# Kernel optimization log

Hardware: AMD Instinct MI355X
Metric: run time of the kernel (lower is better)

Reference implementation:

```python
import jax, jax.numpy as jnp
import numpy as np

N_BLOCKS = 5
D_HIDDEN = 512
D_LATENT = 512
NUM_FREQ = 10
IMG_H = IMG_W = 128


@jax.custom_vjp
def trunc_exp(x):
    return jnp.exp(x)

def _te_fwd(x):
    return jnp.exp(x), x

def _te_bwd(x, g):
    return (g * jnp.exp(jnp.clip(x, -15.0, 15.0)),)

trunc_exp.defvjp(_te_fwd, _te_bwd)


def setup_inputs() -> dict:
    key = jax.random.key(0)
    ks = jax.random.split(key, 12)
    cam, ray, samp = 2, 1024, 48
    world_xyz = jax.random.normal(ks[0], (cam, ray, samp, 3), jnp.float32) * 0.5
    world_xyz = world_xyz.at[..., 2].add(2.5)  # keep points in front of identity camera
    c2w = jnp.tile(jnp.eye(4, dtype=jnp.float32), (cam, 1, 1))
    k_mat = jnp.tile(jnp.array([[128.0, 0.0, 64.0], [0.0, 128.0, 64.0], [0.0, 0.0, 1.0]], jnp.float32), (cam, 1, 1))
    features = jax.random.normal(ks[1], (cam, D_LATENT, IMG_H, IMG_W), jnp.float32)
    s = 0.02
    d_in = 3 + 3 * 2 * NUM_FREQ  # 63
    return {
        'world_xyz': world_xyz,
        'c2w': c2w,
        'k_mat': k_mat,
        'features': features,
        'lin_in_w': jax.random.normal(ks[2], (d_in, D_HIDDEN), jnp.float32) * s,
        'lin_in_b': jnp.zeros((D_HIDDEN,), jnp.float32),
        'lin_z_w': jax.random.normal(ks[3], (N_BLOCKS, D_LATENT, D_HIDDEN), jnp.float32) * s,
        'lin_z_b': jnp.zeros((N_BLOCKS, D_HIDDEN), jnp.float32),
        'fc0_w': jax.random.normal(ks[4], (N_BLOCKS, D_HIDDEN, D_HIDDEN), jnp.float32) * s,
        'fc0_b': jnp.zeros((N_BLOCKS, D_HIDDEN), jnp.float32),
        'fc1_w': jax.random.normal(ks[5], (N_BLOCKS, D_HIDDEN, D_HIDDEN), jnp.float32) * s,
        'fc1_b': jnp.zeros((N_BLOCKS, D_HIDDEN), jnp.float32),
        'lin_out_w': jax.random.normal(ks[6], (D_HIDDEN, 1), jnp.float32) * s,
        'lin_out_b': jnp.zeros((1,), jnp.float32),
    }


def _bilinear(feat, uv):
    # feat: [C, H, W]; uv: [N, 2] pixel coords. Bilinear, border padding, align_corners=True.
    Hd, Wd = feat.shape[1], feat.shape[2]
    x = jnp.clip(uv[:, 0], 0.0, Wd - 1.0)
    y = jnp.clip(uv[:, 1], 0.0, Hd - 1.0)
    x0 = jnp.floor(x); y0 = jnp.floor(y)
    x0i = x0.astype(jnp.int32); y0i = y0.astype(jnp.int32)
    x1i = jnp.minimum(x0i + 1, Wd - 1); y1i = jnp.minimum(y0i + 1, Hd - 1)
    wx = x - x0; wy = y - y0
    f00 = feat[:, y0i, x0i]; f01 = feat[:, y0i, x1i]
    f10 = feat[:, y1i, x0i]; f11 = feat[:, y1i, x1i]
    out = (f00 * ((1 - wx) * (1 - wy)) + f01 * (wx * (1 - wy)) +
           f10 * ((1 - wx) * wy) + f11 * (wx * wy))
    return out.T  # [N, C]


def _forward(world_xyz, c2w, k_mat, features, lin_in_w, lin_in_b, lin_z_w, lin_z_b,
             fc0_w, fc0_b, fc1_w, fc1_b, lin_out_w, lin_out_b):
    B, R, S, _ = world_xyz.shape
    pts = world_xyz.reshape(B, R * S, 3)
    # world -> camera (w2c = inverse of rigid c2w)
    rot = c2w[:, :3, :3]
    trans = c2w[:, :3, 3]
    cam_xyz = jnp.einsum('bji,bnj->bni', rot, pts - trans[:, None])  # R^T (p - t)
    # project with intrinsics
    uvw = jnp.einsum('bij,bnj->bni', k_mat, cam_xyz)
    z = uvw[..., 2:3]
    z = jnp.where(jnp.abs(z) < 1e-6, 1e-6, z)
    uv = uvw[..., :2] / z  # [B, N, 2] pixel coords
    aligned = jax.vmap(_bilinear)(features, uv)  # [B, N, C]
    # NeRF positional encoding (include_input=True, freqs 2^0..2^9, scaled by 2*pi)
    freqs = 2.0 ** jnp.arange(NUM_FREQ, dtype=jnp.float32)
    scaled = (2.0 * jnp.pi) * cam_xyz[..., None] * freqs  # [B, N, 3, F]
    scaled = scaled.reshape(B, R * S, 3 * NUM_FREQ)
    enc = jnp.concatenate([cam_xyz, jnp.sin(scaled), jnp.cos(scaled)], axis=-1)  # [B, N, 63]
    # ResnetFC: lin_in then residual blocks with latent injection
    h = enc @ lin_in_w + lin_in_b
    for i in range(N_BLOCKS):
        h = h + aligned @ lin_z_w[i] + lin_z_b[i]
        net = jax.nn.relu(h) @ fc0_w[i] + fc0_b[i]
        dx = jax.nn.relu(net) @ fc1_w[i] + fc1_b[i]
        h = h + dx
    sigma = jax.nn.relu(h) @ lin_out_w + lin_out_b  # [B, N, 1]
    return trunc_exp(sigma).reshape(B, R, S, 1)


def reference(world_xyz, c2w, k_mat, features, lin_in_w, lin_in_b, lin_z_w, lin_z_b,
              fc0_w, fc0_b, fc1_w, fc1_b, lin_out_w, lin_out_b):
    return _forward(world_xyz, c2w, k_mat, features, lin_in_w, lin_in_b, lin_z_w, lin_z_b,
                    fc0_w, fc0_b, fc1_w, fc1_b, lin_out_w, lin_out_b)
```

## Files before the change

kernel.cpp:

```cpp
#include <hip/hip_runtime.h>

typedef __bf16 bf16_t;
typedef bf16_t bf16x8 __attribute__((ext_vector_type(8)));
typedef float f32x4 __attribute__((ext_vector_type(4)));
typedef unsigned short u16;

#define P_TOTAL 98304
#define PTS_PER_BATCH 49152

__device__ __forceinline__ u16 f2bs(float f){ bf16_t b=(bf16_t)f; return __builtin_bit_cast(u16,b); }

__device__ __forceinline__ void bar_lds(){
  asm volatile("s_waitcnt lgkmcnt(0)" ::: "memory");
  __builtin_amdgcn_s_barrier();
  __builtin_amdgcn_sched_barrier(0);
}

__global__ void k_wtrans15(const float* __restrict__ lz, const float* __restrict__ f0,
                           const float* __restrict__ f1, u16* __restrict__ dst){
  int kt = blockIdx.x, ns = blockIdx.y, z = blockIdx.z;
  const float* src = (z<5) ? (lz + (size_t)z*262144)
                   : (z<10 ? (f0 + (size_t)(z-5)*262144)
                           : (f1 + (size_t)(z-10)*262144));
  u16* d = dst + (size_t)z*262144 + (size_t)(ns*16 + kt)*1024;
  int l = threadIdx.x;
  int col = ns*32 + (l&15);
  int kr  = kt*32 + (l>>4)*8;
  #pragma unroll
  for (int nt=0;nt<2;nt++){
    bf16x8 o;
    #pragma unroll
    for (int j=0;j<8;j++) o[j] = (bf16_t)src[(size_t)(kr+j)*512 + col + nt*16];
    *(bf16x8*)(d + nt*512 + l*8) = o;
  }
}

__global__ void k_wtrans_in(const float* __restrict__ w, u16* __restrict__ dst){
  int kt = blockIdx.x, ns = blockIdx.y;
  u16* d = dst + (size_t)(ns*2 + kt)*1024;
  int l = threadIdx.x;
  int col = ns*32 + (l&15);
  int kr  = kt*32 + (l>>4)*8;
  #pragma unroll
  for (int nt=0;nt<2;nt++){
    bf16x8 o;
    #pragma unroll
    for (int j=0;j<8;j++){
      int k = kr + j;
      o[j] = (k < 63) ? (bf16_t)w[(size_t)k*512 + col + nt*16] : (bf16_t)0.f;
    }
    *(bf16x8*)(d + nt*512 + l*8) = o;
  }
}

__global__ void k_featT(const float* __restrict__ feat, u16* __restrict__ featT){
  int x = threadIdx.x;
  int c8 = blockIdx.x*8;
  int y = blockIdx.y, b = blockIdx.z;
  float v[8];
  #pragma unroll
  for (int j=0;j<8;j++)
    v[j] = feat[(((size_t)(b*512 + c8 + j))*128 + y)*128 + x];
  bf16x8 o;
  #pragma unroll
  for (int j=0;j<8;j++) o[j] = (bf16_t)v[j];
  *(bf16x8*)(featT + (((size_t)(b*128 + y))*128 + x)*512 + c8) = o;
}

__global__ __launch_bounds__(1024) void k_points(
    const float* __restrict__ world, const float* __restrict__ c2w,
    const float* __restrict__ kmat, const u16* __restrict__ featT,
    u16* __restrict__ alignedF, u16* __restrict__ encF){
  __shared__ u16 act[16*520];
  __shared__ u16 encs[16*72];
  int wid = threadIdx.x >> 6, lane = threadIdx.x & 63;
  int p0 = blockIdx.x*16;
  int gp = p0 + wid;
  int b = gp / PTS_PER_BATCH;
  const float* wp = world + (size_t)gp*3;
  float px = wp[0], py = wp[1], pz = wp[2];
  const float* cw = c2w + b*16;
  float dx = px - cw[3], dy = py - cw[7], dz = pz - cw[11];
  float cx = cw[0]*dx + cw[4]*dy + cw[8]*dz;
  float cy = cw[1]*dx + cw[5]*dy + cw[9]*dz;
  float cz = cw[2]*dx + cw[6]*dy + cw[10]*dz;
  const float* km = kmat + b*9;
  float u0 = km[0]*cx + km[1]*cy + km[2]*cz;
  float v0 = km[3]*cx + km[4]*cy + km[5]*cz;
  float zz = km[6]*cx + km[7]*cy + km[8]*cz;
  if (fabsf(zz) < 1e-6f) zz = 1e-6f;
  float uu = u0/zz, vv = v0/zz;
  float xf = fminf(fmaxf(uu, 0.f), 127.f);
  float yf = fminf(fmaxf(vv, 0.f), 127.f);
  float x0f = floorf(xf), y0f = floorf(yf);
  int x0 = (int)x0f, y0 = (int)y0f;
  int x1 = min(x0+1,127), y1 = min(y0+1,127);
  float wx = xf - x0f, wy = yf - y0f;
  float w00 = (1.f-wx)*(1.f-wy), w01 = wx*(1.f-wy), w10 = (1.f-wx)*wy, w11 = wx*wy;
  size_t fb = (size_t)b*128*128*512;
  int c8 = lane*8;
  const bf16x8 t00 = *(const bf16x8*)(featT + fb + (size_t)(y0*128+x0)*512 + c8);
  const bf16x8 t01 = *(const bf16x8*)(featT + fb + (size_t)(y0*128+x1)*512 + c8);
  const bf16x8 t10 = *(const bf16x8*)(featT + fb + (size_t)(y1*128+x0)*512 + c8);
  const bf16x8 t11 = *(const bf16x8*)(featT + fb + (size_t)(y1*128+x1)*512 + c8);
  bf16x8 o;
  #pragma unroll
  for (int j=0;j<8;j++){
    float r = (float)t00[j]*w00 + (float)t01[j]*w01 + (float)t10[j]*w10 + (float)t11[j]*w11;
    o[j] = (bf16_t)r;
  }
  *(bf16x8*)&act[wid*520 + lane*8] = o;
  float cam[3] = {cx, cy, cz};
  float e;
  if (lane < 3) e = cam[lane];
  else if (lane < 33){
    int i = (lane-3)/10, f = (lane-3)%10;
    e = sinf(6.2831855f * cam[i] * (float)(1<<f));
  } else if (lane < 63){
    int i = (lane-33)/10, f = (lane-33)%10;
    e = cosf(6.2831855f * cam[i] * (float)(1<<f));
  } else e = 0.f;
  encs[wid*72 + lane] = f2bs(e);
  __syncthreads();
  int t = threadIdx.x;
  int g = blockIdx.x & 3;
  size_t blk = (size_t)(blockIdx.x >> 2);
  {
    int kt = t>>6, lo = t&63, fm = lo&15, fk8 = lo>>4;
    bf16x8 v = *(const bf16x8*)&act[fm*520 + kt*32 + fk8*8];
    *(bf16x8*)(alignedF + blk*32768 + (size_t)(kt*4+g)*512 + lo*8) = v;
  }
  if (t < 128){
    int kt = t>>6, lo = t&63, fm = lo&15, fk8 = lo>>4;
    bf16x8 v = *(const bf16x8*)&encs[fm*72 + kt*32 + fk8*8];
    *(bf16x8*)(encF + blk*4096 + (size_t)(kt*4+g)*512 + lo*8) = v;
  }
}


#define MFMA_BF16 __builtin_amdgcn_mfma_f32_16x16x32_bf16

template<int NK>
__device__ __forceinline__ void gemm3(const u16* sB, const u16* __restrict__ apS,
                                      const u16* __restrict__ apN,
                                      int l, f32x4 (&acc)[4][4], bf16x8 (&a)[2][4]){
  const u16* bp = sB + l*8;
  bf16x8 br[2][4];
  #pragma unroll
  for (int bt=0; bt<4; ++bt) br[0][bt] = *(const bf16x8*)(bp + bt*512);
  #pragma unroll 1
  for (int kb=0; kb<NK/2-1; ++kb){
    #pragma unroll
    for (int d=0; d<2; ++d){
      const int kt = kb*2 + d;
      #pragma unroll
      for (int bt=0; bt<4; ++bt)
        br[d^1][bt] = *(const bf16x8*)(bp + (kt+1)*2048 + bt*512);
      #pragma unroll
      for (int bt=0; bt<4; ++bt){
        acc[bt][0] = MFMA_BF16(a[d][0], br[d][bt], acc[bt][0], 0,0,0);
        acc[bt][1] = MFMA_BF16(a[d][1], br[d][bt], acc[bt][1], 0,0,0);
        acc[bt][2] = MFMA_BF16(a[d][2], br[d][bt], acc[bt][2], 0,0,0);
        acc[bt][3] = MFMA_BF16(a[d][3], br[d][bt], acc[bt][3], 0,0,0);
      }
      #pragma unroll
      for (int nt=0; nt<4; ++nt)
        a[d][nt] = *(const bf16x8*)(apS + (nt>>1)*(NK*1024) + (kt+2)*1024 + (nt&1)*512);
    }
  }
  #pragma unroll
  for (int d=0; d<2; ++d){
    if (d == 0){
      #pragma unroll
      for (int bt=0; bt<4; ++bt)
        br[1][bt] = *(const bf16x8*)(bp + (NK-1)*2048 + bt*512);
    }
    #pragma unroll
    for (int bt=0; bt<4; ++bt){
      acc[bt][0] = MFMA_BF16(a[d][0], br[d][bt], acc[bt][0], 0,0,0);
      acc[bt][1] = MFMA_BF16(a[d][1], br[d][bt], acc[bt][1], 0,0,0);
      acc[bt][2] = MFMA_BF16(a[d][2], br[d][bt], acc[bt][2], 0,0,0);
      acc[bt][3] = MFMA_BF16(a[d][3], br[d][bt], acc[bt][3], 0,0,0);
    }
    #pragma unroll
    for (int nt=0; nt<4; ++nt)
      a[d][nt] = *(const bf16x8*)(apN + (nt>>1)*16384 + d*1024 + (nt&1)*512);
  }
}

__device__ __forceinline__ void add_bias2(const float* __restrict__ bias, int wn64, int rq,
                                          f32x4 (&acc)[4][4]){
  #pragma unroll
  for (int nt=0; nt<4; ++nt){
    f32x4 bv = *(const f32x4*)&bias[wn64 + nt*16 + rq];
    #pragma unroll
    for (int bt=0; bt<4; ++bt)
      #pragma unroll
      for (int r=0; r<4; ++r)
        acc[bt][nt][r] += bv[r];
  }
}

__device__ __forceinline__ void write_relu3(u16* dst, int w, int fm, int fk8,
                                            f32x4 (&acc)[4][4]){
  u16* base = dst + w*4096 + (fk8>>1)*128 + fm*8 + (fk8&1)*4;
  #pragma unroll
  for (int bt=0; bt<4; ++bt)
    #pragma unroll
    for (int nt=0; nt<4; ++nt){
      u16 p0 = f2bs(fmaxf(acc[bt][nt][0], 0.f));
      u16 p1 = f2bs(fmaxf(acc[bt][nt][1], 0.f));
      u16 p2 = f2bs(fmaxf(acc[bt][nt][2], 0.f));
      u16 p3 = f2bs(fmaxf(acc[bt][nt][3], 0.f));
      uint2 v;
      v.x = (unsigned)p0 | ((unsigned)p1 << 16);
      v.y = (unsigned)p2 | ((unsigned)p3 << 16);
      *(uint2*)(base + (nt>>1)*2048 + (nt&1)*256 + bt*512) = v;
    }
}

__global__ __launch_bounds__(512, 2) void k_net(
    const u16* __restrict__ alignedF, const u16* __restrict__ encF,
    const u16* __restrict__ wtin, const float* __restrict__ b_in,
    const u16* __restrict__ wts, const float* __restrict__ bz,
    const float* __restrict__ b0, const float* __restrict__ b1,
    const float* __restrict__ wout, const float* __restrict__ bout,
    float* __restrict__ out)
{
  __shared__ u16 bufA[32768];
  __shared__ u16 bufB[32768];
  const int t = threadIdx.x, w = t>>6, l = t&63;
  const int wn64 = w*64, fm = l&15, fk8 = l>>4, rq = (l>>4)*4;

  uint4 sa[8];
  const uint4* srcA = (const uint4*)(alignedF + (size_t)blockIdx.x*32768);
  #pragma unroll
  for (int j=0;j<8;j++) sa[j] = srcA[j*512 + t];
  uint4 sb = *((const uint4*)(encF + (size_t)blockIdx.x*4096) + t);

  const u16* apE = wtin + (size_t)w*4096 + l*8;
  bf16x8 afr[2][4];
  #pragma unroll
  for (int d=0; d<2; ++d)
    #pragma unroll
    for (int nt=0; nt<4; ++nt)
      afr[d][nt] = *(const bf16x8*)(apE + (nt>>1)*2048 + d*1024 + (nt&1)*512);

  #pragma unroll
  for (int j=0;j<8;j++) *((uint4*)bufA + j*512 + t) = sa[j];
  *((uint4*)bufB + t) = sb;
  bar_lds();

  const u16* apz0 = wts + (size_t)w*32768 + l*8;
  f32x4 h[4][4] = {};
  gemm3<2>(bufB, apE, apz0, l, h, afr);
  add_bias2(b_in, wn64, rq, h);

  #pragma unroll 1
  for (int i=0;i<5;i++){
    const u16* apz  = wts + (size_t)i*262144      + (size_t)w*32768 + l*8;
    const u16* apf0 = wts + (size_t)(5+i)*262144  + (size_t)w*32768 + l*8;
    const u16* apf1 = wts + (size_t)(10+i)*262144 + (size_t)w*32768 + l*8;
    const u16* apzn = (i<4) ? (wts + (size_t)(i+1)*262144 + (size_t)w*32768 + l*8) : apE;

    gemm3<16>(bufA, apz, apf0, l, h, afr);
    add_bias2(bz + i*512, wn64, rq, h);
    bar_lds();
    write_relu3(bufB, w, fm, fk8, h);
    bar_lds();
    f32x4 acc[4][4] = {};
    gemm3<16>(bufB, apf0, apf1, l, acc, afr);
    add_bias2(b0 + i*512, wn64, rq, acc);
    bar_lds();
    write_relu3(bufB, w, fm, fk8, acc);
    bar_lds();
    gemm3<16>(bufB, apf1, apzn, l, h, afr);
    add_bias2(b1 + i*512, wn64, rq, h);
  }

  float s[4];
  {
    #pragma unroll
    for (int bt=0; bt<4; ++bt) s[bt] = 0.f;
    #pragma unroll
    for (int nt=0; nt<4; ++nt){
      f32x4 wv = *(const f32x4*)&wout[wn64 + nt*16 + rq];
      #pragma unroll
      for (int bt=0; bt<4; ++bt)
        #pragma unroll
        for (int r=0; r<4; ++r)
          s[bt] += fmaxf(h[bt][nt][r], 0.f) * wv[r];
    }
  }
  #pragma unroll
  for (int bt=0; bt<4; ++bt){
    s[bt] += __shfl_xor(s[bt], 16, 64);
    s[bt] += __shfl_xor(s[bt], 32, 64);
  }
  bar_lds();
  float* red = (float*)bufB;
  if (l < 16){
    #pragma unroll
    for (int bt=0; bt<4; ++bt)
      red[w*64 + bt*16 + l] = s[bt];
  }
  bar_lds();
  if (t < 64){
    float a = bout[0];
    #pragma unroll
    for (int wv=0; wv<8; wv++) a += red[wv*64 + t];
    out[blockIdx.x*64 + t] = expf(a);
  }
}

extern "C" void kernel_launch(void* const* d_in, const int* in_sizes, int n_in,
                              void* d_out, int out_size, void* d_ws, size_t ws_size,
                              hipStream_t stream) {
  const float* world = (const float*)d_in[0];
  const float* c2w   = (const float*)d_in[1];
  const float* kmat  = (const float*)d_in[2];
  const float* feat  = (const float*)d_in[3];
  const float* w_in  = (const float*)d_in[4];
  const float* b_in  = (const float*)d_in[5];
  const float* w_z   = (const float*)d_in[6];
  const float* b_z   = (const float*)d_in[7];
  const float* w_f0  = (const float*)d_in[8];
  const float* b_f0  = (const float*)d_in[9];
  const float* w_f1  = (const float*)d_in[10];
  const float* b_f1  = (const float*)d_in[11];
  const float* w_out = (const float*)d_in[12];
  const float* b_out = (const float*)d_in[13];
  float* out = (float*)d_out;
  char* ws = (char*)d_ws;

  size_t off = 0;
  u16* wts   = (u16*)(ws + off); off += (size_t)15*262144*2;
  u16* wtin  = (u16*)(ws + off); off += (size_t)512*64*2;
  u16* featT = (u16*)(ws + off); off += (size_t)2*128*128*512*2;
  u16* alignedF = (u16*)(ws + off); off += (size_t)P_TOTAL*512*2;
  u16* encF  = (u16*)(ws + off); off += (size_t)P_TOTAL*64*2;

  k_wtrans15<<<dim3(16,16,15), 64, 0, stream>>>(w_z, w_f0, w_f1, wts);
  k_wtrans_in<<<dim3(2,16,1), 64, 0, stream>>>(w_in, wtin);
  k_featT<<<dim3(64,128,2), 128, 0, stream>>>(feat, featT);
  k_points<<<dim3(P_TOTAL/16), 1024, 0, stream>>>(world, c2w, kmat, featT, alignedF, encF);
  k_net<<<dim3(P_TOTAL/64), 512, 0, stream>>>(alignedF, encF, wtin, b_in, wts,
      b_z, b_f0, b_f1, w_out, b_out, out);
}
```

Before: 839.5 us.

## Split MLP across 16 waves per block with staggered K order and MFMA priority

Doubles the k_net block to 1024 threads so each of 16 waves owns 32 output columns instead of 64, which halves per-wave accumulators and weight fragments. Each half of the waves starts its K loop at a different offset, so they read different LDS rows and weight rows and contend less. MFMA groups are wrapped in s_setprio to favour matrix issue. The cost is more barrier participants per block and less register reuse per wave. Launch bounds of 1024 threads with 4 blocks per CU may not fit alongside 128KB of LDS per block.

```diff
diff --git a/kernel.cpp b/kernel.cpp
--- a/kernel.cpp
+++ b/kernel.cpp
@@ -141,58 +141,103 @@
 #define MFMA_BF16 __builtin_amdgcn_mfma_f32_16x16x32_bf16
 
 template<int NK>
-__device__ __forceinline__ void gemm3(const u16* sB, const u16* __restrict__ apS,
-                                      const u16* __restrict__ apN,
-                                      int l, f32x4 (&acc)[4][4], bf16x8 (&a)[2][4]){
+__device__ __forceinline__ void gemm4(const u16* sB, const u16* __restrict__ apS,
+                                      const u16* __restrict__ apN, int l, int START,
+                                      f32x4 (&acc)[4][2], bf16x8 (&a)[2][2]){
   const u16* bp = sB + l*8;
-  bf16x8 br[2][4];
-  #pragma unroll
-  for (int bt=0; bt<4; ++bt) br[0][bt] = *(const bf16x8*)(bp + bt*512);
+  constexpr int M = NK - 1;
+  int c0 = START & M;
+  bf16x8 br0 = *(const bf16x8*)(bp + c0*2048);
+  bf16x8 br1 = *(const bf16x8*)(bp + c0*2048 + 512);
+  bf16x8 br2 = *(const bf16x8*)(bp + c0*2048 + 1024);
+  bf16x8 br3 = *(const bf16x8*)(bp + c0*2048 + 1536);
   #pragma unroll 1
-  for (int kb=0; kb<NK/2-1; ++kb){
-    #pragma unroll
-    for (int d=0; d<2; ++d){
-      const int kt = kb*2 + d;
-      #pragma unroll
-      for (int bt=0; bt<4; ++bt)
-        br[d^1][bt] = *(const bf16x8*)(bp + (kt+1)*2048 + bt*512);
-      #pragma unroll
-      for (int bt=0; bt<4; ++bt){
-        acc[bt][0] = MFMA_BF16(a[d][0], br[d][bt], acc[bt][0], 0,0,0);
-        acc[bt][1] = MFMA_BF16(a[d][1], br[d][bt], acc[bt][1], 0,0,0);
-        acc[bt][2] = MFMA_BF16(a[d][2], br[d][bt], acc[bt][2], 0,0,0);
-        acc[bt][3] = MFMA_BF16(a[d][3], br[d][bt], acc[bt][3], 0,0,0);
-      }
-      #pragma unroll
-      for (int nt=0; nt<4; ++nt)
-        a[d][nt] = *(const bf16x8*)(apS + (nt>>1)*(NK*1024) + (kt+2)*1024 + (nt&1)*512);
-    }
-  }
-  #pragma unroll
-  for (int d=0; d<2; ++d){
-    if (d == 0){
-      #pragma unroll
-      for (int bt=0; bt<4; ++bt)
-        br[1][bt] = *(const bf16x8*)(bp + (NK-1)*2048 + bt*512);
-    }
-    #pragma unroll
-    for (int bt=0; bt<4; ++bt){
-      acc[bt][0] = MFMA_BF16(a[d][0], br[d][bt], acc[bt][0], 0,0,0);
-      acc[bt][1] = MFMA_BF16(a[d][1], br[d][bt], acc[bt][1], 0,0,0);
-      acc[bt][2] = MFMA_BF16(a[d][2], br[d][bt], acc[bt][2], 0,0,0);
-      acc[bt][3] = MFMA_BF16(a[d][3], br[d][bt], acc[bt][3], 0,0,0);
-    }
-    #pragma unroll
-    for (int nt=0; nt<4; ++nt)
-      a[d][nt] = *(const bf16x8*)(apN + (nt>>1)*16384 + d*1024 + (nt&1)*512);
-  }
-}
-
-__device__ __forceinline__ void add_bias2(const float* __restrict__ bias, int wn64, int rq,
-                                          f32x4 (&acc)[4][4]){
-  #pragma unroll
-  for (int nt=0; nt<4; ++nt){
-    f32x4 bv = *(const f32x4*)&bias[wn64 + nt*16 + rq];
+  for (int ib=0; ib<NK/2-1; ++ib){
+    {
+      const int i = 2*ib;
+      __builtin_amdgcn_s_setprio(1);
+      acc[0][0] = MFMA_BF16(a[0][0], br0, acc[0][0], 0,0,0);
+      acc[0][1] = MFMA_BF16(a[0][1], br0, acc[0][1], 0,0,0);
+      acc[1][0] = MFMA_BF16(a[0][0], br1, acc[1][0], 0,0,0);
+      acc[1][1] = MFMA_BF16(a[0][1], br1, acc[1][1], 0,0,0);
+      acc[2][0] = MFMA_BF16(a[0][0], br2, acc[2][0], 0,0,0);
+      acc[2][1] = MFMA_BF16(a[0][1], br2, acc[2][1], 0,0,0);
+      acc[3][0] = MFMA_BF16(a[0][0], br3, acc[3][0], 0,0,0);
+      acc[3][1] = MFMA_BF16(a[0][1], br3, acc[3][1], 0,0,0);
+      __builtin_amdgcn_s_setprio(0);
+      int cn = (START + i + 1) & M;
+      br0 = *(const bf16x8*)(bp + cn*2048);
+      br1 = *(const bf16x8*)(bp + cn*2048 + 512);
+      br2 = *(const bf16x8*)(bp + cn*2048 + 1024);
+      br3 = *(const bf16x8*)(bp + cn*2048 + 1536);
+      int ca = (START + i + 2) & M;
+      a[0][0] = *(const bf16x8*)(apS + ca*1024);
+      a[0][1] = *(const bf16x8*)(apS + ca*1024 + 512);
+    }
+    {
+      const int i = 2*ib + 1;
+      __builtin_amdgcn_s_setprio(1);
+      acc[0][0] = MFMA_BF16(a[1][0], br0, acc[0][0], 0,0,0);
+      acc[0][1] = MFMA_BF16(a[1][1], br0, acc[0][1], 0,0,0);
+      acc[1][0] = MFMA_BF16(a[1][0], br1, acc[1][0], 0,0,0);
+      acc[1][1] = MFMA_BF16(a[1][1], br1, acc[1][1], 0,0,0);
+      acc[2][0] = MFMA_BF16(a[1][0], br2, acc[2][0], 0,0,0);
+      acc[2][1] = MFMA_BF16(a[1][1], br2, acc[2][1], 0,0,0);
+      acc[3][0] = MFMA_BF16(a[1][0], br3, acc[3][0], 0,0,0);
+      acc[3][1] = MFMA_BF16(a[1][1], br3, acc[3][1], 0,0,0);
+      __builtin_amdgcn_s_setprio(0);
+      int cn = (START + i + 1) & M;
+      br0 = *(const bf16x8*)(bp + cn*2048);
+      br1 = *(const bf16x8*)(bp + cn*2048 + 512);
+      br2 = *(const bf16x8*)(bp + cn*2048 + 1024);
+      br3 = *(const bf16x8*)(bp + cn*2048 + 1536);
+      int ca = (START + i + 2) & M;
+      a[1][0] = *(const bf16x8*)(apS + ca*1024);
+      a[1][1] = *(const bf16x8*)(apS + ca*1024 + 512);
+    }
+  }
+  {
+    __builtin_amdgcn_s_setprio(1);
+    acc[0][0] = MFMA_BF16(a[0][0], br0, acc[0][0], 0,0,0);
+    acc[0][1] = MFMA_BF16(a[0][1], br0, acc[0][1], 0,0,0);
+    acc[1][0] = MFMA_BF16(a[0][0], br1, acc[1][0], 0,0,0);
+    acc[1][1] = MFMA_BF16(a[0][1], br1, acc[1][1], 0,0,0);
+    acc[2][0] = MFMA_BF16(a[0][0], br2, acc[2][0], 0,0,0);
+    acc[2][1] = MFMA_BF16(a[0][1], br2, acc[2][1], 0,0,0);
+    acc[3][0] = MFMA_BF16(a[0][0], br3, acc[3][0], 0,0,0);
+    acc[3][1] = MFMA_BF16(a[0][1], br3, acc[3][1], 0,0,0);
+    __builtin_amdgcn_s_setprio(0);
+    int cn = (START + NK - 1) & M;
+    br0 = *(const bf16x8*)(bp + cn*2048);
+    br1 = *(const bf16x8*)(bp + cn*2048 + 512);
+    br2 = *(const bf16x8*)(bp + cn*2048 + 1024);
+    br3 = *(const bf16x8*)(bp + cn*2048 + 1536);
+    int ca = START & 15;
+    a[0][0] = *(const bf16x8*)(apN + ca*1024);
+    a[0][1] = *(const bf16x8*)(apN + ca*1024 + 512);
+  }
+  {
+    __builtin_amdgcn_s_setprio(1);
+    acc[0][0] = MFMA_BF16(a[1][0], br0, acc[0][0], 0,0,0);
+    acc[0][1] = MFMA_BF16(a[1][1], br0, acc[0][1], 0,0,0);
+    acc[1][0] = MFMA_BF16(a[1][0], br1, acc[1][0], 0,0,0);
+    acc[1][1] = MFMA_BF16(a[1][1], br1, acc[1][1], 0,0,0);
+    acc[2][0] = MFMA_BF16(a[1][0], br2, acc[2][0], 0,0,0);
+    acc[2][1] = MFMA_BF16(a[1][1], br2, acc[2][1], 0,0,0);
+    acc[3][0] = MFMA_BF16(a[1][0], br3, acc[3][0], 0,0,0);
+    acc[3][1] = MFMA_BF16(a[1][1], br3, acc[3][1], 0,0,0);
+    __builtin_amdgcn_s_setprio(0);
+    int ca = (START + 1) & 15;
+    a[1][0] = *(const bf16x8*)(apN + ca*1024);
+    a[1][1] = *(const bf16x8*)(apN + ca*1024 + 512);
+  }
+}
+
+__device__ __forceinline__ void add_bias4(const float* __restrict__ bias, int wn32, int rq,
+                                          f32x4 (&acc)[4][2]){
+  #pragma unroll
+  for (int nt=0; nt<2; ++nt){
+    f32x4 bv = *(const f32x4*)&bias[wn32 + nt*16 + rq];
     #pragma unroll
     for (int bt=0; bt<4; ++bt)
       #pragma unroll
@@ -201,13 +246,13 @@
   }
 }
 
-__device__ __forceinline__ void write_relu3(u16* dst, int w, int fm, int fk8,
-                                            f32x4 (&acc)[4][4]){
-  u16* base = dst + w*4096 + (fk8>>1)*128 + fm*8 + (fk8&1)*4;
+__device__ __forceinline__ void write_relu4(u16* dst, int w, int fm, int fk8,
+                                            f32x4 (&acc)[4][2]){
+  u16* base = dst + w*2048 + (fk8>>1)*128 + fm*8 + (fk8&1)*4;
   #pragma unroll
   for (int bt=0; bt<4; ++bt)
     #pragma unroll
-    for (int nt=0; nt<4; ++nt){
+    for (int nt=0; nt<2; ++nt){
       u16 p0 = f2bs(fmaxf(acc[bt][nt][0], 0.f));
       u16 p1 = f2bs(fmaxf(acc[bt][nt][1], 0.f));
       u16 p2 = f2bs(fmaxf(acc[bt][nt][2], 0.f));
@@ -215,11 +260,11 @@
       uint2 v;
       v.x = (unsigned)p0 | ((unsigned)p1 << 16);
       v.y = (unsigned)p2 | ((unsigned)p3 << 16);
-      *(uint2*)(base + (nt>>1)*2048 + (nt&1)*256 + bt*512) = v;
-    }
-}
-
-__global__ __launch_bounds__(512, 2) void k_net(
+      *(uint2*)(base + bt*512 + nt*256) = v;
+    }
+}
+
+__global__ __launch_bounds__(1024, 4) void k_net(
     const u16* __restrict__ alignedF, const u16* __restrict__ encF,
     const u16* __restrict__ wtin, const float* __restrict__ b_in,
     const u16* __restrict__ wts, const float* __restrict__ bz,
@@ -230,52 +275,55 @@
   __shared__ u16 bufA[32768];
   __shared__ u16 bufB[32768];
   const int t = threadIdx.x, w = t>>6, l = t&63;
-  const int wn64 = w*64, fm = l&15, fk8 = l>>4, rq = (l>>4)*4;
-
-  uint4 sa[8];
+  const int fm = l&15, fk8 = l>>4, rq = fk8*4;
+  const int wn32 = w*32;
+  const int START = (w>>3) << 3;
+
+  uint4 sa[4];
   const uint4* srcA = (const uint4*)(alignedF + (size_t)blockIdx.x*32768);
   #pragma unroll
-  for (int j=0;j<8;j++) sa[j] = srcA[j*512 + t];
-  uint4 sb = *((const uint4*)(encF + (size_t)blockIdx.x*4096) + t);
-
-  const u16* apE = wtin + (size_t)w*4096 + l*8;
-  bf16x8 afr[2][4];
-  #pragma unroll
-  for (int d=0; d<2; ++d)
-    #pragma unroll
-    for (int nt=0; nt<4; ++nt)
-      afr[d][nt] = *(const bf16x8*)(apE + (nt>>1)*2048 + d*1024 + (nt&1)*512);
-
-  #pragma unroll
-  for (int j=0;j<8;j++) *((uint4*)bufA + j*512 + t) = sa[j];
-  *((uint4*)bufB + t) = sb;
+  for (int j=0;j<4;j++) sa[j] = srcA[j*1024 + t];
+  uint4 sb = {0,0,0,0};
+  const uint4* srcE = (const uint4*)(encF + (size_t)blockIdx.x*4096);
+  if (t < 512) sb = srcE[t];
+
+  const u16* apEl = wtin + (size_t)w*2048 + l*8;
+  bf16x8 a[2][2];
+  #pragma unroll
+  for (int d=0; d<2; ++d){
+    a[d][0] = *(const bf16x8*)(apEl + d*1024);
+    a[d][1] = *(const bf16x8*)(apEl + d*1024 + 512);
+  }
+
+  #pragma unroll
+  for (int j=0;j<4;j++) *((uint4*)bufA + j*1024 + t) = sa[j];
+  if (t < 512) *((uint4*)bufB + t) = sb;
   bar_lds();
 
-  const u16* apz0 = wts + (size_t)w*32768 + l*8;
-  f32x4 h[4][4] = {};
-  gemm3<2>(bufB, apE, apz0, l, h, afr);
-  add_bias2(b_in, wn64, rq, h);
+  f32x4 h[4][2] = {};
+  gemm4<2>(bufB, apEl, wts + (size_t)w*16384 + l*8, l, START, h, a);
+  add_bias4(b_in, wn32, rq, h);
 
   #pragma unroll 1
   for (int i=0;i<5;i++){
-    const u16* apz  = wts + (size_t)i*262144      + (size_t)w*32768 + l*8;
-    const u16* apf0 = wts + (size_t)(5+i)*262144  + (size_t)w*32768 + l*8;
-    const u16* apf1 = wts + (size_t)(10+i)*262144 + (size_t)w*32768 + l*8;
-    const u16* apzn = (i<4) ? (wts + (size_t)(i+1)*262144 + (size_t)w*32768 + l*8) : apE;
-
-    gemm3<16>(bufA, apz, apf0, l, h, afr);
-    add_bias2(bz + i*512, wn64, rq, h);
+    const u16* apz  = wts + (size_t)i*262144      + (size_t)w*16384 + l*8;
+    const u16* apf0 = wts + (size_t)(5+i)*262144  + (size_t)w*16384 + l*8;
+    const u16* apf1 = wts + (size_t)(10+i)*262144 + (size_t)w*16384 + l*8;
+    const u16* apzn = (i<4) ? (wts + (size_t)(i+1)*262144 + (size_t)w*16384 + l*8) : apEl;
+
+    gemm4<16>(bufA, apz, apf0, l, START, h, a);
+    add_bias4(bz + i*512, wn32, rq, h);
     bar_lds();
-    write_relu3(bufB, w, fm, fk8, h);
+    write_relu4(bufB, w, fm, fk8, h);
     bar_lds();
-    f32x4 acc[4][4] = {};
-    gemm3<16>(bufB, apf0, apf1, l, acc, afr);
-    add_bias2(b0 + i*512, wn64, rq, acc);
+    f32x4 acc[4][2] = {};
+    gemm4<16>(bufB, apf0, apf1, l, START, acc, a);
+    add_bias4(b0 + i*512, wn32, rq, acc);
     bar_lds();
-    write_relu3(bufB, w, fm, fk8, acc);
+    write_relu4(bufB, w, fm, fk8, acc);
     bar_lds();
-    gemm3<16>(bufB, apf1, apzn, l, h, afr);
-    add_bias2(b1 + i*512, wn64, rq, h);
+    gemm4<16>(bufB, apf1, apzn, l, START, h, a);
+    add_bias4(b1 + i*512, wn32, rq, h);
   }
 
   float s[4];
@@ -283,8 +331,8 @@
     #pragma unroll
     for (int bt=0; bt<4; ++bt) s[bt] = 0.f;
     #pragma unroll
-    for (int nt=0; nt<4; ++nt){
-      f32x4 wv = *(const f32x4*)&wout[wn64 + nt*16 + rq];
+    for (int nt=0; nt<2; ++nt){
+      f32x4 wv = *(const f32x4*)&wout[wn32 + nt*16 + rq];
       #pragma unroll
       for (int bt=0; bt<4; ++bt)
         #pragma unroll
@@ -306,10 +354,10 @@
   }
   bar_lds();
   if (t < 64){
-    float a = bout[0];
-    #pragma unroll
-    for (int wv=0; wv<8; wv++) a += red[wv*64 + t];
-    out[blockIdx.x*64 + t] = expf(a);
+    float aa = bout[0];
+    #pragma unroll
+    for (int wv=0; wv<16; wv++) aa += red[wv*64 + t];
+    out[blockIdx.x*64 + t] = expf(aa);
   }
 }
 
@@ -344,6 +392,6 @@
   k_wtrans_in<<<dim3(2,16,1), 64, 0, stream>>>(w_in, wtin);
   k_featT<<<dim3(64,128,2), 128, 0, stream>>>(feat, featT);
   k_points<<<dim3(P_TOTAL/16), 1024, 0, stream>>>(world, c2w, kmat, featT, alignedF, encF);
-  k_net<<<dim3(P_TOTAL/64), 512, 0, stream>>>(alignedF, encF, wtin, b_in, wts,
+  k_net<<<dim3(P_TOTAL/64), 1024, 0, stream>>>(alignedF, encF, wtin, b_in, wts,
       b_z, b_f0, b_f1, w_out, b_out, out);
 }
```

New measurement: 857.9 us. 2.2% more time.
